# Optimization experiments

Measured on AMD Instinct MI355X. Metric: run time of the kernel, lower is better.

Reference implementation:

```python
import jax, jax.numpy as jnp
import numpy as np
from jax import lax

EPS = 1e-5
DN = ('NCHW', 'OIHW', 'NCHW')


def setup_inputs() -> dict:
    key = jax.random.key(0)
    ks = jax.random.split(key, 16)
    B = 8192
    # uniform(0,1): every pixel nonzero => all voxels active => sparse conv == dense conv
    x = jax.random.uniform(ks[0], (B, 1, 28, 28), dtype=jnp.float32)

    def conv_params(kw, kb, c_in, c_out, k):
        scale = 1.0 / np.sqrt(c_in * k * k)
        w = jax.random.normal(kw, (c_out, c_in, k, k), dtype=jnp.float32) * scale
        b = jax.random.normal(kb, (c_out,), dtype=jnp.float32) * scale
        return w, b

    w0, b0 = conv_params(ks[1], ks[2], 1, 32, 3)
    w1, b1 = conv_params(ks[3], ks[4], 32, 64, 2)
    w2, b2 = conv_params(ks[5], ks[6], 64, 128, 2)
    # BatchNorm affine params (init: gamma=1, beta=0)
    g0, be0 = jnp.ones((32,), jnp.float32), jnp.zeros((32,), jnp.float32)
    g1, be1 = jnp.ones((64,), jnp.float32), jnp.zeros((64,), jnp.float32)
    g2, be2 = jnp.ones((128,), jnp.float32), jnp.zeros((128,), jnp.float32)
    w_fc = jax.random.normal(ks[7], (10, 128), dtype=jnp.float32) * (1.0 / np.sqrt(128))
    b_fc = jax.random.normal(ks[8], (10,), dtype=jnp.float32) * (1.0 / np.sqrt(128))
    return dict(x=x, w0=w0, b0=b0, g0=g0, be0=be0,
                w1=w1, b1=b1, g1=g1, be1=be1,
                w2=w2, b2=b2, g2=g2, be2=be2,
                w_fc=w_fc, b_fc=b_fc)


def _conv_bn_relu(x, w, b, g, be, stride, padding):
    # sparse conv on fully-active grid == dense conv
    y = lax.conv_general_dilated(x, w, (stride, stride), padding,
                                 dimension_numbers=DN)
    y = y + b[None, :, None, None]
    # BatchNorm1d over (N_active, C) == stats over batch+spatial (biased var)
    mean = jnp.mean(y, axis=(0, 2, 3))
    var = jnp.var(y, axis=(0, 2, 3))
    y = (y - mean[None, :, None, None]) * lax.rsqrt(var + EPS)[None, :, None, None]
    y = y * g[None, :, None, None] + be[None, :, None, None]
    return jax.nn.relu(y)


def reference(x, w0, b0, g0, be0, w1, b1, g1, be1, w2, b2, g2, be2, w_fc, b_fc):
    h = _conv_bn_relu(x, w0, b0, g0, be0, 1, 'SAME')    # (B,32,28,28)
    h = _conv_bn_relu(h, w1, b1, g1, be1, 2, 'VALID')   # (B,64,14,14)
    h = _conv_bn_relu(h, w2, b2, g2, be2, 2, 'VALID')   # (B,128,7,7)
    pooled = jnp.mean(h, axis=(2, 3))                    # AdaptiveAvgPool2d(1)+Flatten
    return pooled @ w_fc.T + b_fc                        # (B, n_classes)
```

## Files before the change

kernel.cpp:

```cpp
#include <hip/hip_runtime.h>
#include <hip/hip_bf16.h>

typedef __bf16 bf16x8 __attribute__((ext_vector_type(8)));
typedef float  f32x4  __attribute__((ext_vector_type(4)));

#define BSZ 8192

union BW2 { __bf16 b[2]; unsigned int u; };
union FR  { unsigned int u[4]; bf16x8 v; };

__global__ __launch_bounds__(256) void k_stats0(const float* __restrict__ x,
                                                float* __restrict__ part0,
                                                const float* __restrict__ w1,
                                                const float* __restrict__ w2,
                                                __bf16* __restrict__ w1b,
                                                __bf16* __restrict__ w2b) {
    __shared__ float xs[900];
    __shared__ float sred[4 * 54];
    const int tid = threadIdx.x;
    {
        int t = blockIdx.x * 256 + tid;
        if (t < 8192) {
            int oc = t >> 7, k = t & 127, c = k & 31, d = k >> 5;
            w1b[t] = (__bf16)w1[oc * 128 + c * 4 + d];
        }
        if (t < 32768) {
            int oc = t >> 8, k = t & 255, c = k & 63, d = k >> 6;
            w2b[t] = (__bf16)w2[oc * 256 + c * 4 + d];
        }
    }
    float a[54];
#pragma unroll
    for (int i = 0; i < 54; i++) a[i] = 0.f;
    for (int i = tid; i < 900; i += 256) xs[i] = 0.f;
    for (int img = 0; img < 8; img++) {
        const float* xb = x + ((long)blockIdx.x * 8 + img) * 784;
        __syncthreads();
        for (int j = tid; j < 784; j += 256) {
            int yy = j / 28, xx = j - yy * 28;
            xs[(yy + 1) * 30 + xx + 1] = xb[j];
        }
        __syncthreads();
        for (int pix = tid; pix < 784; pix += 256) {
            int y = pix / 28, xx = pix - y * 28;
            const float* p = &xs[y * 30 + xx];
            float nv[9];
#pragma unroll
            for (int dy = 0; dy < 3; dy++)
#pragma unroll
                for (int dx = 0; dx < 3; dx++)
                    nv[dy * 3 + dx] = p[dy * 30 + dx];
            int idx = 0;
#pragma unroll
            for (int t2 = 0; t2 < 9; t2++) {
                float vt = nv[t2];
                a[45 + t2] += vt;
#pragma unroll
                for (int u = t2; u < 9; u++) { a[idx] = fmaf(vt, nv[u], a[idx]); idx++; }
            }
        }
    }
#pragma unroll
    for (int i = 0; i < 54; i++) {
        float v = a[i];
        v += __shfl_xor(v, 1);  v += __shfl_xor(v, 2);  v += __shfl_xor(v, 4);
        v += __shfl_xor(v, 8);  v += __shfl_xor(v, 16); v += __shfl_xor(v, 32);
        a[i] = v;
    }
    const int l = tid & 63, w = tid >> 6;
    __syncthreads();
    if (l == 0) {
#pragma unroll
        for (int i = 0; i < 54; i++) sred[w * 54 + i] = a[i];
    }
    __syncthreads();
    if (tid < 54)
        part0[blockIdx.x * 64 + tid] = sred[tid] + sred[54 + tid] + sred[108 + tid] + sred[162 + tid];
}

__global__ void k_fin0(const float* __restrict__ part0, const float* __restrict__ w0,
                       const float* __restrict__ g0, const float* __restrict__ be0,
                       __bf16* __restrict__ wcv) {
    __shared__ float red[4 * 54];
    int t = threadIdx.x, c = t & 63, g = t >> 6;
    if (c < 54) {
        float acc = 0.f;
        for (int i = g; i < 1024; i += 4) acc += part0[i * 64 + c];
        red[g * 54 + c] = acc;
    }
    __syncthreads();
    if (t < 54) red[t] = red[t] + red[54 + t] + red[108 + t] + red[162 + t];
    __syncthreads();
    if (t < 32) {
        float wv[9];
#pragma unroll
        for (int tap = 0; tap < 9; tap++) wv[tap] = w0[t * 9 + tap];
        float sum = 0.f, sq = 0.f;
        int idx = 0;
#pragma unroll
        for (int ta = 0; ta < 9; ta++) {
            sum = fmaf(wv[ta], red[45 + ta], sum);
#pragma unroll
            for (int u = ta; u < 9; u++) {
                float coef = (u == ta) ? 1.f : 2.f;
                sq = fmaf(coef * wv[ta] * wv[u], red[idx], sq);
                idx++;
            }
        }
        float cnt = (float)BSZ * 784.f;
        float mean = sum / cnt;
        float var = sq / cnt - mean * mean;
        float A = g0[t] * rsqrtf(var + 1e-5f);
        float bias = be0[t] - mean * A;
        __bf16 bhi = (__bf16)bias;
        float blo = bias - (float)bhi;
        int nn = t >> 1, hh = t & 1;
#pragma unroll
        for (int qq = 0; qq < 4; qq++) {
#pragma unroll
            for (int e = 0; e < 8; e++) {
                float v = 0.f;
                if (qq < 3) {
                    if (e < 6) {
                        int i = e >> 1;
                        v = (float)((__bf16)(A * wv[qq * 3 + i]));
                    } else if (e == 6) {
                        float wf = A * wv[qq * 3 + 0]; v = wf - (float)((__bf16)wf);
                    } else {
                        float wf = A * wv[qq * 3 + 1]; v = wf - (float)((__bf16)wf);
                    }
                } else {
                    if (e == 0)      { float wf = A * wv[2]; v = wf - (float)((__bf16)wf); }
                    else if (e == 1) { float wf = A * wv[5]; v = wf - (float)((__bf16)wf); }
                    else if (e == 2) { float wf = A * wv[8]; v = wf - (float)((__bf16)wf); }
                    else if (e == 4) v = (float)bhi;
                    else if (e == 5) v = blo;
                }
                wcv[hh * 512 + qq * 128 + nn * 8 + e] = (__bf16)v;
            }
        }
    }
}

struct C0S {
    bf16x8 bwM0, bwM1;
    int q, n;
    int Koff, off1, off2;
    bool q3;
};

__device__ inline void c0_init(C0S& S, const __bf16* __restrict__ wcv, int l) {
    S.q = l >> 4; S.n = l & 15; S.q3 = (S.q == 3);
    S.bwM0 = *(const bf16x8*)&wcv[S.q * 128 + S.n * 8];
    S.bwM1 = *(const bf16x8*)&wcv[512 + S.q * 128 + S.n * 8];
    S.Koff = S.q3 ? 2 : S.q * 30;
    S.off1 = S.q3 ? 30 : 1;
    S.off2 = S.q3 ? 60 : 2;
}

__device__ inline void c0_produce(const C0S& S, const unsigned* __restrict__ xs2w,
                                  __bf16* dst, int my, int mx, bool zpad) {
    const int b00 = 2 * my * 30 + 2 * mx + S.Koff;
#pragma unroll
    for (int t = 0; t < 4; t++) {
        const int d1 = t >> 1, d0 = t & 1;
        const unsigned* p = xs2w + b00 + d1 * 30 + d0;
        unsigned v0 = p[0], v1 = p[S.off1], v2 = p[S.off2];
        unsigned pm = __builtin_amdgcn_perm(v1, v0, 0x05040100u);
        FR A;
        A.u[0] = S.q3 ? pm : v0;
        A.u[1] = S.q3 ? (v2 & 0xffffu) : v1;
        A.u[2] = S.q3 ? 0x3F803F80u : v2;
        A.u[3] = S.q3 ? 0u : pm;
        f32x4 z = {0.f, 0.f, 0.f, 0.f};
        f32x4 ac0 = __builtin_amdgcn_mfma_f32_16x16x32_bf16(A.v, S.bwM0, z, 0, 0, 0);
        f32x4 ac1 = __builtin_amdgcn_mfma_f32_16x16x32_bf16(A.v, S.bwM1, z, 0, 0, 0);
#pragma unroll
        for (int r = 0; r < 4; r++) {
            float a0 = fmaxf(ac0[r], 0.f), a1 = fmaxf(ac1[r], 0.f);
            if (zpad) { a0 = 0.f; a1 = 0.f; }
            BW2 pk; pk.b[0] = (__bf16)a0; pk.b[1] = (__bf16)a1;
            *(unsigned*)&dst[(S.q * 4 + r) * 136 + t * 32 + 2 * S.n] = pk.u;
        }
    }
}

__device__ inline void stage_img(unsigned* xs2w, const float* __restrict__ x,
                                 long b, int t0, int stride) {
    for (int jj = t0; jj < 784; jj += stride) {
        int yy = jj / 28, xx2 = jj - yy * 28;
        float f = x[b * 784 + jj];
        __bf16 hi = (__bf16)f;
        __bf16 lo = (__bf16)(f - (float)hi);
        BW2 pk; pk.b[0] = hi; pk.b[1] = lo;
        xs2w[(yy + 1) * 30 + xx2 + 1] = pk.u;
    }
}

__global__ __launch_bounds__(256, 3) void k_conv01(const float* __restrict__ x,
                                                   const __bf16* __restrict__ wcv,
                                                   const __bf16* __restrict__ w1b,
                                                   __bf16* __restrict__ h1,
                                                   float* __restrict__ part1) {
    __shared__ unsigned xs2a[4][900];
    __shared__ __attribute__((aligned(16))) __bf16 sAta[4][2][16 * 136];
    const int tid = threadIdx.x, w = tid >> 6, l = tid & 63;
    const int q = l >> 4, n = l & 15;
    unsigned* xs2w = xs2a[w];
    C0S S0; c0_init(S0, wcv, l);
    bf16x8 fbv[4][4];
#pragma unroll
    for (int g = 0; g < 4; g++)
#pragma unroll
        for (int kc = 0; kc < 4; kc++)
            fbv[g][kc] = *(const bf16x8*)&w1b[(4 * n + g) * 128 + kc * 32 + q * 8];
    const long b = (long)blockIdx.x * 4 + w;
    for (int i = l; i < 900; i += 64) xs2w[i] = 0u;
    stage_img(xs2w, x, b, l, 64);
    float ssum[4] = {0.f, 0.f, 0.f, 0.f}, ssq[4] = {0.f, 0.f, 0.f, 0.f};
    __bf16* hb = h1 + b * 12544;

    auto prod = [&](int mt) {
        const bool last = (mt == 12);
        int mv = (last && n >= 4) ? 195 : mt * 16 + n;
        int my = mv / 14, mx = mv - my * 14;
        c0_produce(S0, xs2w, sAta[w][mt & 1], my, mx, last && (q != 0));
    };

    prod(0);
    for (int mt = 0; mt < 13; mt++) {
        if (mt < 12) prod(mt + 1);
        const __bf16* sa = &sAta[w][mt & 1][n * 136 + q * 8];
        bf16x8 fav[4];
#pragma unroll
        for (int kc = 0; kc < 4; kc++) fav[kc] = *(const bf16x8*)&sa[kc * 32];
        f32x4 a[4];
        __builtin_amdgcn_s_setprio(1);
#pragma unroll
        for (int g = 0; g < 4; g++) {
            f32x4 acc = {0.f, 0.f, 0.f, 0.f};
#pragma unroll
            for (int kc = 0; kc < 4; kc++)
                acc = __builtin_amdgcn_mfma_f32_16x16x32_bf16(fav[kc], fbv[g][kc], acc, 0, 0, 0);
            a[g] = acc;
        }
        __builtin_amdgcn_s_setprio(0);
#pragma unroll
        for (int g = 0; g < 4; g++)
#pragma unroll
            for (int r = 0; r < 4; r++) {
                ssum[g] += a[g][r];
                ssq[g] = fmaf(a[g][r], a[g][r], ssq[g]);
            }
        if ((mt < 12) | (q == 0)) {
#pragma unroll
            for (int r = 0; r < 4; r++) {
                BW2 p0, p1v;
                p0.b[0] = (__bf16)a[0][r]; p0.b[1] = (__bf16)a[1][r];
                p1v.b[0] = (__bf16)a[2][r]; p1v.b[1] = (__bf16)a[3][r];
                uint2 u; u.x = p0.u; u.y = p1v.u;
                *(uint2*)&hb[(mt * 16 + q * 4 + r) * 64 + 4 * n] = u;
            }
        }
    }
#pragma unroll
    for (int g = 0; g < 4; g++) {
        ssum[g] += __shfl_xor(ssum[g], 16); ssum[g] += __shfl_xor(ssum[g], 32);
        ssq[g]  += __shfl_xor(ssq[g], 16);  ssq[g]  += __shfl_xor(ssq[g], 32);
    }
    if (l < 16) {
#pragma unroll
        for (int g = 0; g < 4; g++) {
            part1[(long)(4 * l + g) * BSZ + b] = ssum[g];
            part1[(long)(64 + 4 * l + g) * BSZ + b] = ssq[g];
        }
    }
}

__global__ __launch_bounds__(256) void k_redfin(const float* __restrict__ part,
                                                const float* __restrict__ g,
                                                const float* __restrict__ be,
                                                float* __restrict__ abc,
                                                int C, float cnt) {
    __shared__ float s1[256], s2[256];
    const int c = blockIdx.x, tid = threadIdx.x;
    float a = 0.f, bq = 0.f;
    const float* p1 = part + (long)c * BSZ;
    const float* p2 = part + (long)(C + c) * BSZ;
    for (int i = tid; i < BSZ; i += 256) { a += p1[i]; bq += p2[i]; }
    s1[tid] = a; s2[tid] = bq;
    __syncthreads();
    for (int s = 128; s > 0; s >>= 1) {
        if (tid < s) { s1[tid] += s1[tid + s]; s2[tid] += s2[tid + s]; }
        __syncthreads();
    }
    if (tid == 0) {
        float mean = s1[0] / cnt;
        float var = s2[0] / cnt - mean * mean;
        float A = g[c] * rsqrtf(var + 1e-5f);
        abc[c] = A;
        abc[C + c] = be[c] - mean * A;
    }
}

__global__ __launch_bounds__(256) void k_conv2s(__bf16* __restrict__ h1,
                                                const __bf16* __restrict__ w2b,
                                                const float* __restrict__ abc1,
                                                float* __restrict__ part2) {
    __shared__ __attribute__((aligned(16))) __bf16 sAt[2][16 * 264];
    __shared__ float sbn1[128];
    const int tid = threadIdx.x;
    if (tid < 128) sbn1[tid] = abc1[tid];
    const int w = tid >> 6, l = tid & 63, q = l >> 4, n = l & 15;
    bf16x8 fbv[2][8];
#pragma unroll
    for (int ntl = 0; ntl < 2; ntl++) {
        int oc = w * 32 + 2 * n + ntl;
#pragma unroll
        for (int kc = 0; kc < 8; kc++)
            fbv[ntl][kc] = *(const bf16x8*)&w2b[oc * 256 + kc * 32 + q * 8];
    }
    const int rlA = tid >> 5, rlB = 8 + (tid >> 5), oo = (tid & 31) * 8;
    const int dA = oo >> 6, cA = oo & 63;

    auto issue = [&](int li, bf16x8& A0, bf16x8& A1) {
        const int img = li >> 2, mt = li & 3;
        const __bf16* src = h1 + ((long)blockIdx.x * 4 + img) * 12544;
        int r0 = mt * 16 + rlA;
        if (r0 < 49) {
            int py = r0 / 7, px = r0 - py * 7;
            int msrc = (2 * py + (dA >> 1)) * 14 + 2 * px + (dA & 1);
            A0 = *(const bf16x8*)&src[msrc * 64 + cA];
        }
        int r1 = mt * 16 + rlB;
        if (r1 < 49) {
            int py = r1 / 7, px = r1 - py * 7;
            int msrc = (2 * py + (dA >> 1)) * 14 + 2 * px + (dA & 1);
            A1 = *(const bf16x8*)&src[msrc * 64 + cA];
        }
    };
    auto put = [&](int li, bf16x8 A0, bf16x8 A1) {
        const int mt = li & 3;
        __bf16* sb = sAt[li & 1];
        bf16x8 wv;
        if (mt * 16 + rlA < 49) {
#pragma unroll
            for (int j = 0; j < 8; j++)
                wv[j] = (__bf16)fmaxf((float)A0[j] * sbn1[cA + j] + sbn1[64 + cA + j], 0.f);
        } else {
#pragma unroll
            for (int j = 0; j < 8; j++) wv[j] = (__bf16)0.0f;
        }
        *(bf16x8*)&sb[rlA * 264 + oo] = wv;
        if (mt * 16 + rlB < 49) {
#pragma unroll
            for (int j = 0; j < 8; j++)
                wv[j] = (__bf16)fmaxf((float)A1[j] * sbn1[cA + j] + sbn1[64 + cA + j], 0.f);
        } else {
#pragma unroll
            for (int j = 0; j < 8; j++) wv[j] = (__bf16)0.0f;
        }
        *(bf16x8*)&sb[rlB * 264 + oo] = wv;
    };

    bf16x8 pA0 = {}, pA1 = {}, pB0 = {}, pB1 = {}, pC0 = {}, pC1 = {};
    issue(0, pA0, pA1);
    issue(1, pB0, pB1);
    __syncthreads();
    float ssum[2] = {0.f, 0.f}, ssq[2] = {0.f, 0.f};
    for (int li = 0; li < 16; li++) {
        const int img = li >> 2, mt = li & 3;
        put(li, pA0, pA1);
        if (li < 14) issue(li + 2, pC0, pC1);
        __builtin_amdgcn_sched_barrier(0);
        asm volatile("s_waitcnt lgkmcnt(0)" ::: "memory");
        __builtin_amdgcn_s_barrier();
        __builtin_amdgcn_sched_barrier(0);
        const __bf16* sb = sAt[li & 1];
        bf16x8 fav[8];
#pragma unroll
        for (int kc = 0; kc < 8; kc++)
            fav[kc] = *(const bf16x8*)&sb[n * 264 + kc * 32 + q * 8];
        f32x4 accA = {0.f, 0.f, 0.f, 0.f}, accB = {0.f, 0.f, 0.f, 0.f};
        __builtin_amdgcn_s_setprio(1);
#pragma unroll
        for (int kc = 0; kc < 8; kc++) {
            accA = __builtin_amdgcn_mfma_f32_16x16x32_bf16(fav[kc], fbv[0][kc], accA, 0, 0, 0);
            accB = __builtin_amdgcn_mfma_f32_16x16x32_bf16(fav[kc], fbv[1][kc], accB, 0, 0, 0);
        }
        __builtin_amdgcn_s_setprio(0);
        __bf16* src = h1 + ((long)blockIdx.x * 4 + img) * 12544;
#pragma unroll
        for (int rr = 0; rr < 4; rr++) {
            int m = mt * 16 + q * 4 + rr;
            BW2 pk; pk.b[0] = (__bf16)accA[rr]; pk.b[1] = (__bf16)accB[rr];
            if (m < 49) *(unsigned int*)&src[m * 128 + w * 32 + 2 * n] = pk.u;
            ssum[0] += accA[rr]; ssq[0] = fmaf(accA[rr], accA[rr], ssq[0]);
            ssum[1] += accB[rr]; ssq[1] = fmaf(accB[rr], accB[rr], ssq[1]);
        }
        pA0 = pB0; pA1 = pB1; pB0 = pC0; pB1 = pC1;
        if (mt == 3) {
            const long b = (long)blockIdx.x * 4 + img;
#pragma unroll
            for (int ntl = 0; ntl < 2; ntl++) {
                ssum[ntl] += __shfl_xor(ssum[ntl], 16); ssum[ntl] += __shfl_xor(ssum[ntl], 32);
                ssq[ntl]  += __shfl_xor(ssq[ntl], 16);  ssq[ntl]  += __shfl_xor(ssq[ntl], 32);
            }
            if (l < 16) {
#pragma unroll
                for (int ntl = 0; ntl < 2; ntl++) {
                    int oc = w * 32 + 2 * l + ntl;
                    part2[(long)oc * BSZ + b] = ssum[ntl];
                    part2[(long)(128 + oc) * BSZ + b] = ssq[ntl];
                }
            }
            ssum[0] = ssum[1] = ssq[0] = ssq[1] = 0.f;
        }
    }
}

__global__ __launch_bounds__(256) void k_final(const __bf16* __restrict__ z2,
                                               const float* __restrict__ abc2,
                                               const float* __restrict__ wfc,
                                               const float* __restrict__ bfc,
                                               float* __restrict__ out) {
    const int tid = threadIdx.x, w = tid >> 6, l = tid & 63;
    const int q = l >> 4, g = l & 15;
    const long b = (long)blockIdx.x * 4 + w;
    const __bf16* src = z2 + b * 12544;
    f32x4 a2lo = *(const f32x4*)&abc2[g * 8];
    f32x4 a2hi = *(const f32x4*)&abc2[g * 8 + 4];
    f32x4 b2lo = *(const f32x4*)&abc2[128 + g * 8];
    f32x4 b2hi = *(const f32x4*)&abc2[128 + g * 8 + 4];
    float acc[8];
#pragma unroll
    for (int j = 0; j < 8; j++) acc[j] = 0.f;
    for (int r = q; r < 49; r += 4) {
        bf16x8 v = *(const bf16x8*)&src[r * 128 + g * 8];
#pragma unroll
        for (int j = 0; j < 4; j++) {
            acc[j]     += fmaxf((float)v[j]     * a2lo[j] + b2lo[j], 0.f);
            acc[4 + j] += fmaxf((float)v[4 + j] * a2hi[j] + b2hi[j], 0.f);
        }
    }
#pragma unroll
    for (int j = 0; j < 8; j++) {
        acc[j] += __shfl_xor(acc[j], 16);
        acc[j] += __shfl_xor(acc[j], 32);
        acc[j] *= (1.f / 49.f);
    }
    float p[10];
#pragma unroll
    for (int o = 0; o < 10; o++) {
        f32x4 w0 = *(const f32x4*)&wfc[o * 128 + g * 8];
        f32x4 w1 = *(const f32x4*)&wfc[o * 128 + g * 8 + 4];
        float s = 0.f;
#pragma unroll
        for (int j = 0; j < 4; j++) {
            s = fmaf(acc[j], w0[j], s);
            s = fmaf(acc[4 + j], w1[j], s);
        }
        p[o] = s;
    }
#pragma unroll
    for (int o = 0; o < 10; o++) {
        p[o] += __shfl_xor(p[o], 1); p[o] += __shfl_xor(p[o], 2);
        p[o] += __shfl_xor(p[o], 4); p[o] += __shfl_xor(p[o], 8);
    }
    if (l == 0) {
#pragma unroll
        for (int o = 0; o < 10; o++) out[b * 10 + o] = p[o] + bfc[o];
    }
}

extern "C" void kernel_launch(void* const* d_in, const int* in_sizes, int n_in,
                              void* d_out, int out_size, void* d_ws, size_t ws_size,
                              hipStream_t stream) {
    const float* x   = (const float*)d_in[0];
    const float* w0  = (const float*)d_in[1];
    const float* g0  = (const float*)d_in[3];
    const float* be0 = (const float*)d_in[4];
    const float* w1  = (const float*)d_in[5];
    const float* g1  = (const float*)d_in[7];
    const float* be1 = (const float*)d_in[8];
    const float* w2  = (const float*)d_in[9];
    const float* g2  = (const float*)d_in[11];
    const float* be2 = (const float*)d_in[12];
    const float* wfc = (const float*)d_in[13];
    const float* bfc = (const float*)d_in[14];
    float* out = (float*)d_out;

    float* ws    = (float*)d_ws;
    float* part0 = ws;
    __bf16* wcv  = (__bf16*)(part0 + 1008 * 64);
    float* abc0  = part0 + 1024 * 64;
    float* part1 = abc0 + 320;
    float* abc1  = part1 + 128 * BSZ;
    float* part2 = abc1 + 128;
    float* abc2  = part2 + 256 * BSZ;
    __bf16* w1b  = (__bf16*)(abc2 + 256);
    __bf16* w2b  = w1b + 8192;
    __bf16* h1   = w2b + 32768;

    k_stats0<<<dim3(1024), dim3(256), 0, stream>>>(x, part0, w1, w2, w1b, w2b);
    k_fin0<<<dim3(1), dim3(256), 0, stream>>>(part0, w0, g0, be0, wcv);
    k_conv01<<<dim3(BSZ / 4), dim3(256), 0, stream>>>(x, wcv, w1b, h1, part1);
    k_redfin<<<dim3(64), dim3(256), 0, stream>>>(part1, g1, be1, abc1, 64, (float)(BSZ * 196));
    k_conv2s<<<dim3(BSZ / 4), dim3(256), 0, stream>>>(h1, w2b, abc1, part2);
    k_redfin<<<dim3(128), dim3(256), 0, stream>>>(part2, g2, be2, abc2, 128, (float)(BSZ * 49));
    k_final<<<dim3(BSZ / 4), dim3(256), 0, stream>>>(h1, abc2, wfc, bfc, out);
}
```

Before: 371.0 us.

## Replace BN partial-sum buffers and reduce kernels with replicated atomics

Per-image BN statistics for conv1 and conv2 are now accumulated with atomicAdd into 8 replicated accumulator slots (zeroed in k_stats0), instead of being written to large per-image partial arrays. This removes the two k_redfin launches: the consumer kernels (k_conv2s, k_final) fold the 8 replicas and compute scale and shift in their prologues. Separately, k_conv01 drops the double-buffered A tile for a single buffer, reading fragments before producing the next tile, and raises launch bounds to 4 blocks per SM. The costs are atomic contention on a few addresses, redundant BN finalisation in every block, and a possible hazard from the single buffer if producer writes are not ordered after fragment reads.

New measurement: 418.6 us. +12.8%, slower.

```diff
diff --git a/kernel.cpp b/kernel.cpp
--- a/kernel.cpp
+++ b/kernel.cpp
@@ -14,12 +14,14 @@
                                                 const float* __restrict__ w1,
                                                 const float* __restrict__ w2,
                                                 __bf16* __restrict__ w1b,
-                                                __bf16* __restrict__ w2b) {
+                                                __bf16* __restrict__ w2b,
+                                                float* __restrict__ acc) {
     __shared__ float xs[900];
     __shared__ float sred[4 * 54];
     const int tid = threadIdx.x;
     {
         int t = blockIdx.x * 256 + tid;
+        if (t < 3072) acc[t] = 0.f;
         if (t < 8192) {
             int oc = t >> 7, k = t & 127, c = k & 31, d = k >> 5;
             w1b[t] = (__bf16)w1[oc * 128 + c * 4 + d];
@@ -197,16 +199,17 @@
     }
 }
 
-__global__ __launch_bounds__(256, 3) void k_conv01(const float* __restrict__ x,
+__global__ __launch_bounds__(256, 4) void k_conv01(const float* __restrict__ x,
                                                    const __bf16* __restrict__ wcv,
                                                    const __bf16* __restrict__ w1b,
                                                    __bf16* __restrict__ h1,
-                                                   float* __restrict__ part1) {
+                                                   float* __restrict__ acc1) {
     __shared__ unsigned xs2a[4][900];
-    __shared__ __attribute__((aligned(16))) __bf16 sAta[4][2][16 * 136];
+    __shared__ __attribute__((aligned(16))) __bf16 sAta[4][16 * 136];
     const int tid = threadIdx.x, w = tid >> 6, l = tid & 63;
     const int q = l >> 4, n = l & 15;
     unsigned* xs2w = xs2a[w];
+    __bf16* sAtw = sAta[w];
     C0S S0; c0_init(S0, wcv, l);
     bf16x8 fbv[4][4];
 #pragma unroll
@@ -224,16 +227,16 @@
         const bool last = (mt == 12);
         int mv = (last && n >= 4) ? 195 : mt * 16 + n;
         int my = mv / 14, mx = mv - my * 14;
-        c0_produce(S0, xs2w, sAta[w][mt & 1], my, mx, last && (q != 0));
+        c0_produce(S0, xs2w, sAtw, my, mx, last && (q != 0));
     };
 
     prod(0);
     for (int mt = 0; mt < 13; mt++) {
+        const __bf16* sa = &sAtw[n * 136 + q * 8];
+        bf16x8 fav[4];
+#pragma unroll
+        for (int kc = 0; kc < 4; kc++) fav[kc] = *(const bf16x8*)&sa[kc * 32];
         if (mt < 12) prod(mt + 1);
-        const __bf16* sa = &sAta[w][mt & 1][n * 136 + q * 8];
-        bf16x8 fav[4];
-#pragma unroll
-        for (int kc = 0; kc < 4; kc++) fav[kc] = *(const bf16x8*)&sa[kc * 32];
         f32x4 a[4];
         __builtin_amdgcn_s_setprio(1);
 #pragma unroll
@@ -269,48 +272,39 @@
         ssq[g]  += __shfl_xor(ssq[g], 16);  ssq[g]  += __shfl_xor(ssq[g], 32);
     }
     if (l < 16) {
+        const int rep = (int)((blockIdx.x * 4 + w) & 7);
+        float* ab = acc1 + rep * 128;
 #pragma unroll
         for (int g = 0; g < 4; g++) {
-            part1[(long)(4 * l + g) * BSZ + b] = ssum[g];
-            part1[(long)(64 + 4 * l + g) * BSZ + b] = ssq[g];
-        }
-    }
-}
-
-__global__ __launch_bounds__(256) void k_redfin(const float* __restrict__ part,
-                                                const float* __restrict__ g,
-                                                const float* __restrict__ be,
-                                                float* __restrict__ abc,
-                                                int C, float cnt) {
-    __shared__ float s1[256], s2[256];
-    const int c = blockIdx.x, tid = threadIdx.x;
-    float a = 0.f, bq = 0.f;
-    const float* p1 = part + (long)c * BSZ;
-    const float* p2 = part + (long)(C + c) * BSZ;
-    for (int i = tid; i < BSZ; i += 256) { a += p1[i]; bq += p2[i]; }
-    s1[tid] = a; s2[tid] = bq;
-    __syncthreads();
-    for (int s = 128; s > 0; s >>= 1) {
-        if (tid < s) { s1[tid] += s1[tid + s]; s2[tid] += s2[tid + s]; }
-        __syncthreads();
-    }
-    if (tid == 0) {
-        float mean = s1[0] / cnt;
-        float var = s2[0] / cnt - mean * mean;
-        float A = g[c] * rsqrtf(var + 1e-5f);
-        abc[c] = A;
-        abc[C + c] = be[c] - mean * A;
+            atomicAdd(&ab[4 * l + g], ssum[g]);
+            atomicAdd(&ab[64 + 4 * l + g], ssq[g]);
+        }
     }
 }
 
 __global__ __launch_bounds__(256) void k_conv2s(__bf16* __restrict__ h1,
                                                 const __bf16* __restrict__ w2b,
-                                                const float* __restrict__ abc1,
-                                                float* __restrict__ part2) {
+                                                const float* __restrict__ acc1,
+                                                const float* __restrict__ g1,
+                                                const float* __restrict__ be1,
+                                                float* __restrict__ acc2) {
     __shared__ __attribute__((aligned(16))) __bf16 sAt[2][16 * 264];
     __shared__ float sbn1[128];
     const int tid = threadIdx.x;
-    if (tid < 128) sbn1[tid] = abc1[tid];
+    if (tid < 64) {
+        float s = 0.f, sq = 0.f;
+#pragma unroll
+        for (int r = 0; r < 8; r++) {
+            s += acc1[r * 128 + tid];
+            sq += acc1[r * 128 + 64 + tid];
+        }
+        const float cnt = (float)BSZ * 196.f;
+        float mean = s / cnt;
+        float var = sq / cnt - mean * mean;
+        float A = g1[tid] * rsqrtf(var + 1e-5f);
+        sbn1[tid] = A;
+        sbn1[64 + tid] = be1[tid] - mean * A;
+    }
     const int w = tid >> 6, l = tid & 63, q = l >> 4, n = l & 15;
     bf16x8 fbv[2][8];
 #pragma unroll
@@ -400,18 +394,19 @@
         }
         pA0 = pB0; pA1 = pB1; pB0 = pC0; pB1 = pC1;
         if (mt == 3) {
-            const long b = (long)blockIdx.x * 4 + img;
 #pragma unroll
             for (int ntl = 0; ntl < 2; ntl++) {
                 ssum[ntl] += __shfl_xor(ssum[ntl], 16); ssum[ntl] += __shfl_xor(ssum[ntl], 32);
                 ssq[ntl]  += __shfl_xor(ssq[ntl], 16);  ssq[ntl]  += __shfl_xor(ssq[ntl], 32);
             }
             if (l < 16) {
+                const int rep = (int)((blockIdx.x + img) & 7);
+                float* ab = acc2 + rep * 256;
 #pragma unroll
                 for (int ntl = 0; ntl < 2; ntl++) {
                     int oc = w * 32 + 2 * l + ntl;
-                    part2[(long)oc * BSZ + b] = ssum[ntl];
-                    part2[(long)(128 + oc) * BSZ + b] = ssq[ntl];
+                    atomicAdd(&ab[oc], ssum[ntl]);
+                    atomicAdd(&ab[128 + oc], ssq[ntl]);
                 }
             }
             ssum[0] = ssum[1] = ssq[0] = ssq[1] = 0.f;
@@ -420,18 +415,36 @@
 }
 
 __global__ __launch_bounds__(256) void k_final(const __bf16* __restrict__ z2,
-                                               const float* __restrict__ abc2,
+                                               const float* __restrict__ acc2,
+                                               const float* __restrict__ g2,
+                                               const float* __restrict__ be2,
                                                const float* __restrict__ wfc,
                                                const float* __restrict__ bfc,
                                                float* __restrict__ out) {
+    __shared__ float sbn2[256];
     const int tid = threadIdx.x, w = tid >> 6, l = tid & 63;
+    if (tid < 128) {
+        float s = 0.f, sq = 0.f;
+#pragma unroll
+        for (int r = 0; r < 8; r++) {
+            s += acc2[r * 256 + tid];
+            sq += acc2[r * 256 + 128 + tid];
+        }
+        const float cnt = (float)BSZ * 49.f;
+        float mean = s / cnt;
+        float var = sq / cnt - mean * mean;
+        float A = g2[tid] * rsqrtf(var + 1e-5f);
+        sbn2[tid] = A;
+        sbn2[128 + tid] = be2[tid] - mean * A;
+    }
+    __syncthreads();
     const int q = l >> 4, g = l & 15;
     const long b = (long)blockIdx.x * 4 + w;
     const __bf16* src = z2 + b * 12544;
-    f32x4 a2lo = *(const f32x4*)&abc2[g * 8];
-    f32x4 a2hi = *(const f32x4*)&abc2[g * 8 + 4];
-    f32x4 b2lo = *(const f32x4*)&abc2[128 + g * 8];
-    f32x4 b2hi = *(const f32x4*)&abc2[128 + g * 8 + 4];
+    f32x4 a2lo = *(const f32x4*)&sbn2[g * 8];
+    f32x4 a2hi = *(const f32x4*)&sbn2[g * 8 + 4];
+    f32x4 b2lo = *(const f32x4*)&sbn2[128 + g * 8];
+    f32x4 b2hi = *(const f32x4*)&sbn2[128 + g * 8 + 4];
     float acc[8];
 #pragma unroll
     for (int j = 0; j < 8; j++) acc[j] = 0.f;
@@ -495,6 +508,8 @@
     __bf16* wcv  = (__bf16*)(part0 + 1008 * 64);
     float* abc0  = part0 + 1024 * 64;
     float* part1 = abc0 + 320;
+    float* acc1  = part1;
+    float* acc2  = part1 + 1024;
     float* abc1  = part1 + 128 * BSZ;
     float* part2 = abc1 + 128;
     float* abc2  = part2 + 256 * BSZ;
@@ -502,11 +517,9 @@
     __bf16* w2b  = w1b + 8192;
     __bf16* h1   = w2b + 32768;
 
-    k_stats0<<<dim3(1024), dim3(256), 0, stream>>>(x, part0, w1, w2, w1b, w2b);
+    k_stats0<<<dim3(1024), dim3(256), 0, stream>>>(x, part0, w1, w2, w1b, w2b, acc1);
     k_fin0<<<dim3(1), dim3(256), 0, stream>>>(part0, w0, g0, be0, wcv);
-    k_conv01<<<dim3(BSZ / 4), dim3(256), 0, stream>>>(x, wcv, w1b, h1, part1);
-    k_redfin<<<dim3(64), dim3(256), 0, stream>>>(part1, g1, be1, abc1, 64, (float)(BSZ * 196));
-    k_conv2s<<<dim3(BSZ / 4), dim3(256), 0, stream>>>(h1, w2b, abc1, part2);
-    k_redfin<<<dim3(128), dim3(256), 0, stream>>>(part2, g2, be2, abc2, 128, (float)(BSZ * 49));
-    k_final<<<dim3(BSZ / 4), dim3(256), 0, stream>>>(h1, abc2, wfc, bfc, out);
-}
+    k_conv01<<<dim3(BSZ / 4), dim3(256), 0, stream>>>(x, wcv, w1b, h1, acc1);
+    k_conv2s<<<dim3(BSZ / 4), dim3(256), 0, stream>>>(h1, w2b, acc1, g1, be1, acc2);
+    k_final<<<dim3(BSZ / 4), dim3(256), 0, stream>>>(h1, acc2, g2, be2, wfc, bfc, out);
+}
```
